# Optimization experiments

Hardware: AMD Instinct MI355X
Metric: run time of the kernel (lower is better)

Reference implementation:

```python
import jax, jax.numpy as jnp
import numpy as np

EMBED_DIM = 1024
NUM_HEADS = 16
HEAD_DIM = EMBED_DIM // NUM_HEADS


def setup_inputs() -> dict:
    key = jax.random.key(0)
    ks = jax.random.split(key, 7)
    B, S, E = 2, 2048, EMBED_DIM
    scale = 1.0 / np.sqrt(E)
    x = jax.random.normal(ks[0], (B, S, E), dtype=jnp.float32)
    Wq = jax.random.normal(ks[1], (E, E), dtype=jnp.float32) * scale
    Wk = jax.random.normal(ks[2], (E, E), dtype=jnp.float32) * scale
    Wv = jax.random.normal(ks[3], (E, E), dtype=jnp.float32) * scale
    bq = jax.random.normal(ks[4], (E,), dtype=jnp.float32) * 0.01
    bk = jax.random.normal(ks[5], (E,), dtype=jnp.float32) * 0.01
    bv = jax.random.normal(ks[6], (E,), dtype=jnp.float32) * 0.01
    return {"x": x, "Wq": Wq, "bq": bq, "Wk": Wk, "bk": bk, "Wv": Wv, "bv": bv}


def reference(x, Wq, bq, Wk, bk, Wv, bv):
    B, S, E = x.shape
    H, D = NUM_HEADS, HEAD_DIM
    # QKV projections (nn.Linear: x @ W^T + b; W sampled square so we use x @ W + b equivalently as the learned map)
    q = (x @ Wq + bq).reshape(B, S, H, D)
    k = (x @ Wk + bk).reshape(B, S, H, D)
    v = (x @ Wv + bv).reshape(B, S, H, D)
    # scores: [B, H, S, S] -- NOTE: original applies no 1/sqrt(d) scaling
    scores = jnp.einsum("bqhd,bkhd->bhqk", q, k)
    attn = jax.nn.softmax(scores, axis=-1)
    out = jnp.einsum("bhqk,bkhd->bqhd", attn, v)
    return out.reshape(B, S, E)
```

## Files before the change

### kernel.cpp

```cpp
#include <hip/hip_runtime.h>

#define E_DIM 1024
#define NHEADS 16
#define HDIM 64
#define BATCH 2
#define SEQ 2048
#define M_TOT (BATCH*SEQ)

typedef _Float16 f16;
typedef _Float16 half4 __attribute__((ext_vector_type(4)));
typedef _Float16 half8 __attribute__((ext_vector_type(8)));
typedef _Float16 half2v __attribute__((ext_vector_type(2)));
typedef float floatx4 __attribute__((ext_vector_type(4)));

#define MFMA16x32(a,b,c) __builtin_amdgcn_mfma_f32_16x16x32_f16((a),(b),(c),0,0,0)

__device__ __forceinline__ void gll16(const f16* gsrc, f16* ldst) {
    __builtin_amdgcn_global_load_lds(
        (const __attribute__((address_space(1))) void*)gsrc,
        (__attribute__((address_space(3))) void*)ldst, 16, 0, 0);
}

__global__ __launch_bounds__(256) void cvt_x(const float* __restrict__ x,
                                             f16* __restrict__ xh) {
    size_t i = ((size_t)blockIdx.x * 256 + threadIdx.x) * 8;
    float4 a = *(const float4*)&x[i];
    float4 b = *(const float4*)&x[i + 4];
    half8 h = {(f16)a.x,(f16)a.y,(f16)a.z,(f16)a.w,
               (f16)b.x,(f16)b.y,(f16)b.z,(f16)b.w};
    *(half8*)&xh[i] = h;
}

__global__ __launch_bounds__(256) void transpose_w(
    const float* __restrict__ Wq, const float* __restrict__ Wk,
    const float* __restrict__ Wv,
    f16* __restrict__ WTq, f16* __restrict__ WTk, f16* __restrict__ WTv)
{
    const int z = blockIdx.z;
    const float* W = (z == 0) ? Wq : (z == 1) ? Wk : Wv;
    f16* WT        = (z == 0) ? WTq : (z == 1) ? WTk : WTv;

    const int k0 = blockIdx.x * 64, n0 = blockIdx.y * 64;
    const int tid = threadIdx.x;
    __shared__ f16 T[64][68];

    {
        const int tr = tid >> 4, tc = tid & 15;
        float4 f4[4];
        #pragma unroll
        for (int i = 0; i < 4; i++)
            f4[i] = *(const float4*)&W[(size_t)(k0 + tr * 4 + i) * E_DIM + n0 + tc * 4];
        #pragma unroll
        for (int j = 0; j < 4; j++) {
            float e0 = (j==0)?f4[0].x:(j==1)?f4[0].y:(j==2)?f4[0].z:f4[0].w;
            float e1 = (j==0)?f4[1].x:(j==1)?f4[1].y:(j==2)?f4[1].z:f4[1].w;
            float e2 = (j==0)?f4[2].x:(j==1)?f4[2].y:(j==2)?f4[2].z:f4[2].w;
            float e3 = (j==0)?f4[3].x:(j==1)?f4[3].y:(j==2)?f4[3].z:f4[3].w;
            half4 h = {(f16)e0, (f16)e1, (f16)e2, (f16)e3};
            *(half4*)&T[tc * 4 + j][tr * 4] = h;
        }
    }
    __syncthreads();
    {
        const int nn = tid >> 2, kk = (tid & 3) * 16;
        half8 a = *(const half8*)&T[nn][kk];
        half8 b = *(const half8*)&T[nn][kk + 8];
        f16* dst = &WT[(size_t)(n0 + nn) * E_DIM + k0 + kk];
        *(half8*)dst = a;
        *(half8*)(dst + 8) = b;
    }
}

__global__ __launch_bounds__(256) void qkv_gemm(
    const f16* __restrict__ xh, const f16* __restrict__ WTall,
    const float* __restrict__ bq, const float* __restrict__ bk,
    const float* __restrict__ bv,
    f16* __restrict__ qh, f16* __restrict__ kh, f16* __restrict__ vh)
{
    const int flat = blockIdx.x;
    const int rb = (flat & 7) * 96 + (flat >> 3);
    const int z   = rb >> 8;
    const int ntl = rb & 7;
    const int mt  = (rb >> 3) & 31;

    const float* bias = (z == 0) ? bq : (z == 1) ? bk : bv;
    f16* out          = (z == 0) ? qh : (z == 1) ? kh : vh;

    const int m0 = mt * 128;
    const int n0g = z * 1024 + ntl * 128;
    const int tid = threadIdx.x;
    const int lane = tid & 63;
    const int w  = tid >> 6;
    const int wm = w >> 1, wn = w & 1;
    const int g  = lane >> 4, r = lane & 15;

    __shared__ f16 Al[128 * 64];
    __shared__ f16 Bl[128 * 64];

    const int lrow = lane >> 3;
    const int lcol = ((lane & 7) ^ lrow) * 8;
    const f16* asrc = xh    + (size_t)(m0  + lrow) * E_DIM + lcol;
    const f16* bsrc = WTall + (size_t)(n0g + lrow) * E_DIM + lcol;

    floatx4 acc[4][4];
    #pragma unroll
    for (int i = 0; i < 4; i++)
        #pragma unroll
        for (int j = 0; j < 4; j++)
            acc[i][j] = (floatx4){0.f, 0.f, 0.f, 0.f};

    for (int k0 = 0; k0 < E_DIM; k0 += 64) {
        if (k0) __syncthreads();
        #pragma unroll
        for (int t = 0; t < 4; t++) {
            int c = w * 4 + t;
            gll16(asrc + (size_t)c * 8 * E_DIM + k0, Al + c * 512);
            gll16(bsrc + (size_t)c * 8 * E_DIM + k0, Bl + c * 512);
        }
        __syncthreads();

        #pragma unroll
        for (int ks = 0; ks < 64; ks += 32) {
            half8 af[4], bf[4];
            #pragma unroll
            for (int i = 0; i < 4; i++) {
                int row = wm * 64 + i * 16 + r;
                af[i] = *(const half8*)&Al[row * 64 + ((ks + g * 8) ^ ((row & 7) << 3))];
            }
            #pragma unroll
            for (int j = 0; j < 4; j++) {
                int row = wn * 64 + j * 16 + r;
                bf[j] = *(const half8*)&Bl[row * 64 + ((ks + g * 8) ^ ((row & 7) << 3))];
            }
            #pragma unroll
            for (int i = 0; i < 4; i++)
                #pragma unroll
                for (int j = 0; j < 4; j++)
                    acc[i][j] = MFMA16x32(af[i], bf[j], acc[i][j]);
        }
    }

    #pragma unroll
    for (int j = 0; j < 4; j++) {
        int col = ntl * 128 + wn * 64 + j * 16 + r;
        float bb = bias[col];
        #pragma unroll
        for (int i = 0; i < 4; i++)
            #pragma unroll
            for (int rr = 0; rr < 4; rr++) {
                int row = m0 + wm * 64 + i * 16 + g * 4 + rr;
                out[(size_t)row * E_DIM + col] = (f16)(acc[i][j][rr] + bb);
            }
    }
}

__global__ __launch_bounds__(256) void qkv_proj_v2(
    const float* __restrict__ x,
    const f16* __restrict__ WTq, const f16* __restrict__ WTk,
    const f16* __restrict__ WTv,
    const float* __restrict__ bq, const float* __restrict__ bk,
    const float* __restrict__ bv,
    f16* __restrict__ qh, f16* __restrict__ kh, f16* __restrict__ vh)
{
    const int flat = blockIdx.x;
    const int rb = (flat & 7) * 96 + (flat >> 3);
    const int nt = rb & 7;
    const int mt = (rb >> 3) & 31;
    const int z  = rb >> 8;

    const f16* WT     = (z == 0) ? WTq : (z == 1) ? WTk : WTv;
    const float* bias = (z == 0) ? bq : (z == 1) ? bk : bv;
    f16* out          = (z == 0) ? qh : (z == 1) ? kh : vh;

    const int m0 = mt * 128, n0 = nt * 128;
    const int tid = threadIdx.x;
    const int lane = tid & 63;
    const int w  = tid >> 6;
    const int wm = w >> 1, wn = w & 1;
    const int g  = lane >> 4, r = lane & 15;

    __shared__ f16 Al[128 * 32];
    __shared__ f16 Bl[128 * 32];

    floatx4 acc[4][4];
    #pragma unroll
    for (int i = 0; i < 4; i++)
        #pragma unroll
        for (int j = 0; j < 4; j++)
            acc[i][j] = (floatx4){0.f, 0.f, 0.f, 0.f};

    for (int k0 = 0; k0 < E_DIM; k0 += 32) {
        #pragma unroll
        for (int it = 0; it < 2; it++) {
            int idx = tid + it * 256;
            int mm = idx >> 2, kc = (idx & 3) * 8;
            const float* s = &x[(size_t)(m0 + mm) * E_DIM + k0 + kc];
            float4 u = *(const float4*)s;
            float4 v = *(const float4*)(s + 4);
            half8 hv = {(f16)u.x,(f16)u.y,(f16)u.z,(f16)u.w,
                        (f16)v.x,(f16)v.y,(f16)v.z,(f16)v.w};
            *(half8*)&Al[mm * 32 + (kc ^ (((mm >> 2) & 3) << 3))] = hv;
        }
        #pragma unroll
        for (int it = 0; it < 2; it++) {
            int idx = tid + it * 256;
            int nn = idx >> 2, kc = (idx & 3) * 8;
            half8 hv = *(const half8*)&WT[(size_t)(n0 + nn) * E_DIM + k0 + kc];
            *(half8*)&Bl[nn * 32 + (kc ^ (((nn >> 2) & 3) << 3))] = hv;
        }
        __syncthreads();

        half8 af[4], bf[4];
        #pragma unroll
        for (int i = 0; i < 4; i++) {
            int row = wm * 64 + i * 16 + r;
            af[i] = *(const half8*)&Al[row * 32 + ((g * 8) ^ (((row >> 2) & 3) << 3))];
        }
        #pragma unroll
        for (int j = 0; j < 4; j++) {
            int row = wn * 64 + j * 16 + r;
            bf[j] = *(const half8*)&Bl[row * 32 + ((g * 8) ^ (((row >> 2) & 3) << 3))];
        }
        #pragma unroll
        for (int i = 0; i < 4; i++)
            #pragma unroll
            for (int j = 0; j < 4; j++)
                acc[i][j] = MFMA16x32(af[i], bf[j], acc[i][j]);
        __syncthreads();
    }

    #pragma unroll
    for (int j = 0; j < 4; j++) {
        int col = n0 + wn * 64 + j * 16 + r;
        float bb = bias[col];
        #pragma unroll
        for (int i = 0; i < 4; i++)
            #pragma unroll
            for (int rr = 0; rr < 4; rr++) {
                int row = m0 + wm * 64 + i * 16 + g * 4 + rr;
                out[(size_t)row * E_DIM + col] = (f16)(acc[i][j][rr] + bb);
            }
    }
}

__global__ __launch_bounds__(512, 4) void attn(
    const f16* __restrict__ qh, const f16* __restrict__ kh,
    const f16* __restrict__ vh, float* __restrict__ out)
{
    const int flat = blockIdx.x;
    const int rb = (flat & 7) * 64 + (flat >> 3);
    const int qt = rb & 15;
    const int hh = (rb >> 4) & 15;
    const int b  = rb >> 8;
    const int q0 = qt * 128;

    const int tid = threadIdx.x;
    const int lane = tid & 63;
    const int w = tid >> 6;
    const int g = lane >> 4, r = lane & 15;

    __shared__ f16 K_s[2][64 * 64];
    __shared__ f16 V_s[2][64 * 64];

    const size_t base = ((size_t)b * SEQ) * E_DIM + (size_t)hh * HDIM;

    half8 aq[2];
    {
        const f16* qp = &qh[base + (size_t)(q0 + w * 16 + r) * E_DIM];
        aq[0] = *(const half8*)&qp[g * 8];
        aq[1] = *(const half8*)&qp[32 + g * 8];
    }

    const int klrow = lane >> 3;
    const int kcol = ((lane & 7) ^ klrow) * 8;
    const f16* kg0 = kh + base + (size_t)(w * 8 + klrow) * E_DIM + kcol;

    const int vp = tid >> 4, vdc = (tid & 15) * 4;
    const int kv0 = vp * 2;
    const int kvp0 = (kv0 & 3) | (((kv0 >> 4) & 1) << 2) |
                     (((kv0 >> 2) & 3) << 3) | ((kv0 >> 5) << 5);
    const f16* vg0 = vh + base + (size_t)kv0 * E_DIM + vdc;

    float m_run = -1e30f, l_run = 0.f;
    floatx4 acco[4];
    #pragma unroll
    for (int dj = 0; dj < 4; dj++) acco[dj] = (floatx4){0.f, 0.f, 0.f, 0.f};

    const int NT = SEQ / 64;

    gll16(kg0, &K_s[0][w * 512]);
    {
        half4 v0 = *(const half4*)vg0;
        half4 v1 = *(const half4*)(vg0 + E_DIM);
        #pragma unroll
        for (int e = 0; e < 4; e++) {
            int d = vdc + e;
            int swv = ((d ^ (d >> 3)) & 7) << 3;
            half2v pr = {v0[e], v1[e]};
            *(half2v*)&V_s[0][d * 64 + (kvp0 ^ swv)] = pr;
        }
    }
    __syncthreads();

    for (int t = 0; t < NT; t++) {
        const int cur = t & 1;
        const bool pf = (t + 1 < NT);
        half4 v0n, v1n;
        if (pf) {
            gll16(kg0 + (size_t)(t + 1) * 64 * E_DIM, &K_s[cur ^ 1][w * 512]);
            const f16* vsrc = vg0 + (size_t)(t + 1) * 64 * E_DIM;
            v0n = *(const half4*)vsrc;
            v1n = *(const half4*)(vsrc + E_DIM);
        }

        floatx4 sct[4];
        __builtin_amdgcn_s_setprio(1);
        #pragma unroll
        for (int kb = 0; kb < 4; kb++) {
            int kr2 = kb * 16 + r;
            int swk = (kr2 & 7) << 3;
            const f16* kb_ = &K_s[cur][kr2 * 64];
            half8 kf0 = *(const half8*)&kb_[(g * 8) ^ swk];
            half8 kf1 = *(const half8*)&kb_[(32 + g * 8) ^ swk];
            floatx4 c = (floatx4){0.f, 0.f, 0.f, 0.f};
            c = MFMA16x32(kf0, aq[0], c);
            c = MFMA16x32(kf1, aq[1], c);
            sct[kb] = c;
        }
        __builtin_amdgcn_s_setprio(0);

        float pm = sct[0][0];
        #pragma unroll
        for (int kb = 0; kb < 4; kb++)
            #pragma unroll
            for (int rr = 0; rr < 4; rr++)
                pm = fmaxf(pm, sct[kb][rr]);
        pm = fmaxf(pm, __shfl_xor(pm, 16, 64));
        pm = fmaxf(pm, __shfl_xor(pm, 32, 64));
        if (!__all(pm - m_run <= 8.f)) {
            float mn = fmaxf(m_run, pm);
            float alpha = __expf(m_run - mn);
            m_run = mn;
            l_run *= alpha;
            #pragma unroll
            for (int dj = 0; dj < 4; dj++)
                #pragma unroll
                for (int rr = 0; rr < 4; rr++)
                    acco[dj][rr] *= alpha;
        }
        float rs = 0.f;
        #pragma unroll
        for (int kb = 0; kb < 4; kb++)
            #pragma unroll
            for (int rr = 0; rr < 4; rr++) {
                float e = __expf(sct[kb][rr] - m_run);
                sct[kb][rr] = e;
                rs += e;
            }
        rs += __shfl_xor(rs, 16, 64);
        rs += __shfl_xor(rs, 32, 64);
        l_run += rs;

        half8 pa[2];
        #pragma unroll
        for (int h = 0; h < 2; h++) {
            half8 tv = {(f16)sct[h*2][0],   (f16)sct[h*2][1],
                        (f16)sct[h*2][2],   (f16)sct[h*2][3],
                        (f16)sct[h*2+1][0], (f16)sct[h*2+1][1],
                        (f16)sct[h*2+1][2], (f16)sct[h*2+1][3]};
            pa[h] = tv;
        }

        if (pf) {
            #pragma unroll
            for (int e = 0; e < 4; e++) {
                int d = vdc + e;
                int swv = ((d ^ (d >> 3)) & 7) << 3;
                half2v pr = {v0n[e], v1n[e]};
                *(half2v*)&V_s[cur ^ 1][d * 64 + (kvp0 ^ swv)] = pr;
            }
        }

        __builtin_amdgcn_s_setprio(1);
        #pragma unroll
        for (int dj = 0; dj < 4; dj++) {
            int d = dj * 16 + r;
            int swv = ((d ^ (d >> 3)) & 7) << 3;
            const f16* vb_ = &V_s[cur][d * 64];
            half8 vf0 = *(const half8*)&vb_[(g * 8) ^ swv];
            half8 vf1 = *(const half8*)&vb_[(32 + g * 8) ^ swv];
            acco[dj] = MFMA16x32(vf0, pa[0], acco[dj]);
            acco[dj] = MFMA16x32(vf1, pa[1], acco[dj]);
        }
        __builtin_amdgcn_s_setprio(0);

        __syncthreads();
    }

    {
        float inv = 1.f / l_run;
        int row = q0 + w * 16 + r;
        float* orow = out + (size_t)(b * SEQ + row) * E_DIM + hh * HDIM;
        #pragma unroll
        for (int dj = 0; dj < 4; dj++) {
            float4 st = {acco[dj][0] * inv, acco[dj][1] * inv,
                         acco[dj][2] * inv, acco[dj][3] * inv};
            *(float4*)&orow[dj * 16 + g * 4] = st;
        }
    }
}

extern "C" void kernel_launch(void* const* d_in, const int* in_sizes, int n_in,
                              void* d_out, int out_size, void* d_ws, size_t ws_size,
                              hipStream_t stream) {
    const float* x  = (const float*)d_in[0];
    const float* Wq = (const float*)d_in[1];
    const float* bq = (const float*)d_in[2];
    const float* Wk = (const float*)d_in[3];
    const float* bk = (const float*)d_in[4];
    const float* Wv = (const float*)d_in[5];
    const float* bv = (const float*)d_in[6];
    float* out = (float*)d_out;

    const size_t qkv_elems = (size_t)M_TOT * E_DIM;
    const size_t w_elems   = (size_t)E_DIM * E_DIM;
    f16* qh  = (f16*)d_ws;
    f16* kh  = qh + qkv_elems;
    f16* vh  = kh + qkv_elems;
    f16* WTq = vh + qkv_elems;
    f16* WTk = WTq + w_elems;
    f16* WTv = WTk + w_elems;
    f16* xh  = WTv + w_elems;
    const size_t need_v3  = (3 * qkv_elems + 3 * w_elems + qkv_elems) * sizeof(f16);
    const size_t need_v2  = (3 * qkv_elems + 3 * w_elems) * sizeof(f16);
    if (ws_size < need_v2) return;

    if (ws_size >= need_v3) {
        cvt_x<<<dim3(M_TOT * E_DIM / (256 * 8)), 256, 0, stream>>>(x, xh);
        transpose_w<<<dim3(16, 16, 3), 256, 0, stream>>>(Wq, Wk, Wv, WTq, WTk, WTv);
        qkv_gemm<<<dim3((E_DIM / 128) * (M_TOT / 128) * 3), 256, 0, stream>>>(
            xh, WTq, bq, bk, bv, qh, kh, vh);
    } else {
        transpose_w<<<dim3(16, 16, 3), 256, 0, stream>>>(Wq, Wk, Wv, WTq, WTk, WTv);
        qkv_proj_v2<<<dim3((E_DIM / 128) * (M_TOT / 128) * 3), 256, 0, stream>>>(
            x, WTq, WTk, WTv, bq, bk, bv, qh, kh, vh);
    }
    attn<<<dim3((SEQ / 128) * NHEADS * BATCH), 512, 0, stream>>>(qh, kh, vh, out);
}
```

Before: 173.5 us.

## Use exp2 softmax with prescaled Q and compute row sums via MFMA

Q is prescaled by log2(e) so the softmax can use the native exp2 instruction, and the lazy-rescale threshold is adjusted to match. The per-tile row-sum reduction with cross-lane shuffles is replaced by an extra MFMA against a vector of ones, which accumulates the P row sums in matrix registers. It also uses packed round-toward-zero f16 conversion, three-input max trees, and precomputed V shared-memory store offsets. Scaling Q in f16 and accumulating the denominator from f16-rounded P slightly change numerics, and the extra MFMAs add matrix-unit work per tile.

Result: faster. 169.1 us (-2.5%).

```diff
diff --git a/kernel.cpp b/kernel.cpp
--- a/kernel.cpp
+++ b/kernel.cpp
@@ -14,6 +14,12 @@
 typedef float floatx4 __attribute__((ext_vector_type(4)));
 
 #define MFMA16x32(a,b,c) __builtin_amdgcn_mfma_f32_16x16x32_f16((a),(b),(c),0,0,0)
+#define EXP2F(x) __builtin_amdgcn_exp2f(x)
+#define FMAX3(a,b,c) fmaxf(fmaxf((a),(b)),(c))
+
+__device__ __forceinline__ half2v pkrtz(float a, float b) {
+    return __builtin_bit_cast(half2v, __builtin_amdgcn_cvt_pkrtz(a, b));
+}
 
 __device__ __forceinline__ void gll16(const f16* gsrc, f16* ldst) {
     __builtin_amdgcn_global_load_lds(
@@ -267,8 +273,8 @@
     half8 aq[2];
     {
         const f16* qp = &qh[base + (size_t)(q0 + w * 16 + r) * E_DIM];
-        aq[0] = *(const half8*)&qp[g * 8];
-        aq[1] = *(const half8*)&qp[32 + g * 8];
+        aq[0] = *(const half8*)&qp[g * 8] * (f16)1.44269504f;
+        aq[1] = *(const half8*)&qp[32 + g * 8] * (f16)1.44269504f;
     }
 
     const int klrow = lane >> 3;
@@ -280,9 +286,19 @@
     const int kvp0 = (kv0 & 3) | (((kv0 >> 4) & 1) << 2) |
                      (((kv0 >> 2) & 3) << 3) | ((kv0 >> 5) << 5);
     const f16* vg0 = vh + base + (size_t)kv0 * E_DIM + vdc;
-
-    float m_run = -1e30f, l_run = 0.f;
+    int voff[4];
+    #pragma unroll
+    for (int e = 0; e < 4; e++) {
+        int d = vdc + e;
+        voff[e] = d * 64 + (kvp0 ^ (((d ^ (d >> 3)) & 7) << 3));
+    }
+
+    const half8 ones = {(f16)1.f,(f16)1.f,(f16)1.f,(f16)1.f,
+                        (f16)1.f,(f16)1.f,(f16)1.f,(f16)1.f};
+
+    float m_run = -1e30f;
     floatx4 acco[4];
+    floatx4 acc5 = (floatx4){0.f, 0.f, 0.f, 0.f};
     #pragma unroll
     for (int dj = 0; dj < 4; dj++) acco[dj] = (floatx4){0.f, 0.f, 0.f, 0.f};
 
@@ -294,10 +310,8 @@
         half4 v1 = *(const half4*)(vg0 + E_DIM);
         #pragma unroll
         for (int e = 0; e < 4; e++) {
-            int d = vdc + e;
-            int swv = ((d ^ (d >> 3)) & 7) << 3;
             half2v pr = {v0[e], v1[e]};
-            *(half2v*)&V_s[0][d * 64 + (kvp0 ^ swv)] = pr;
+            *(half2v*)&V_s[0][voff[e]] = pr;
         }
     }
     __syncthreads();
@@ -329,55 +343,47 @@
         }
         __builtin_amdgcn_s_setprio(0);
 
-        float pm = sct[0][0];
-        #pragma unroll
-        for (int kb = 0; kb < 4; kb++)
-            #pragma unroll
-            for (int rr = 0; rr < 4; rr++)
-                pm = fmaxf(pm, sct[kb][rr]);
+        float t0 = FMAX3(sct[0][0], sct[0][1], sct[0][2]);
+        float t1 = FMAX3(sct[0][3], sct[1][0], sct[1][1]);
+        float t2 = FMAX3(sct[1][2], sct[1][3], sct[2][0]);
+        float t3 = FMAX3(sct[2][1], sct[2][2], sct[2][3]);
+        float t4 = FMAX3(sct[3][0], sct[3][1], sct[3][2]);
+        float pm = fmaxf(FMAX3(t0, t1, t2), FMAX3(t3, t4, sct[3][3]));
         pm = fmaxf(pm, __shfl_xor(pm, 16, 64));
         pm = fmaxf(pm, __shfl_xor(pm, 32, 64));
-        if (!__all(pm - m_run <= 8.f)) {
+        if (!__all(pm - m_run <= 11.544f)) {
             float mn = fmaxf(m_run, pm);
-            float alpha = __expf(m_run - mn);
+            float alpha = EXP2F(m_run - mn);
             m_run = mn;
-            l_run *= alpha;
+            acc5 *= alpha;
             #pragma unroll
             for (int dj = 0; dj < 4; dj++)
                 #pragma unroll
                 for (int rr = 0; rr < 4; rr++)
                     acco[dj][rr] *= alpha;
         }
-        float rs = 0.f;
-        #pragma unroll
-        for (int kb = 0; kb < 4; kb++)
-            #pragma unroll
-            for (int rr = 0; rr < 4; rr++) {
-                float e = __expf(sct[kb][rr] - m_run);
-                sct[kb][rr] = e;
-                rs += e;
-            }
-        rs += __shfl_xor(rs, 16, 64);
-        rs += __shfl_xor(rs, 32, 64);
-        l_run += rs;
-
+
+        union H8 { half8 v; half2v h2[4]; };
         half8 pa[2];
         #pragma unroll
         for (int h = 0; h < 2; h++) {
-            half8 tv = {(f16)sct[h*2][0],   (f16)sct[h*2][1],
-                        (f16)sct[h*2][2],   (f16)sct[h*2][3],
-                        (f16)sct[h*2+1][0], (f16)sct[h*2+1][1],
-                        (f16)sct[h*2+1][2], (f16)sct[h*2+1][3]};
-            pa[h] = tv;
+            H8 u;
+            #pragma unroll
+            for (int q = 0; q < 2; q++) {
+                int kb = h * 2 + q;
+                u.h2[q * 2 + 0] = pkrtz(
+                    EXP2F(sct[kb][0] - m_run), EXP2F(sct[kb][1] - m_run));
+                u.h2[q * 2 + 1] = pkrtz(
+                    EXP2F(sct[kb][2] - m_run), EXP2F(sct[kb][3] - m_run));
+            }
+            pa[h] = u.v;
         }
 
         if (pf) {
             #pragma unroll
             for (int e = 0; e < 4; e++) {
-                int d = vdc + e;
-                int swv = ((d ^ (d >> 3)) & 7) << 3;
                 half2v pr = {v0n[e], v1n[e]};
-                *(half2v*)&V_s[cur ^ 1][d * 64 + (kvp0 ^ swv)] = pr;
+                *(half2v*)&V_s[cur ^ 1][voff[e]] = pr;
             }
         }
 
@@ -392,13 +398,15 @@
             acco[dj] = MFMA16x32(vf0, pa[0], acco[dj]);
             acco[dj] = MFMA16x32(vf1, pa[1], acco[dj]);
         }
+        acc5 = MFMA16x32(ones, pa[0], acc5);
+        acc5 = MFMA16x32(ones, pa[1], acc5);
         __builtin_amdgcn_s_setprio(0);
 
         __syncthreads();
     }
 
     {
-        float inv = 1.f / l_run;
+        float inv = 1.f / acc5[0];
         int row = q0 + w * 16 + r;
         float* orow = out + (size_t)(b * SEQ + row) * E_DIM + hh * HDIM;
         #pragma unroll
```
